# Optimization experiments

Measured on AMD Instinct MI355X. Metric: run time of the kernel, lower is better.

## Reference

```python
import jax, jax.numpy as jnp
import numpy as np

GAMMA = 1.0
INPUT_DIM = 512
NUM_CENTERS = 4096
BATCH = 16384


def setup_inputs() -> dict:
    key = jax.random.key(0)
    kx, kc = jax.random.split(key)
    x = jax.random.normal(kx, (BATCH, INPUT_DIM), dtype=jnp.float32)
    centers = jax.random.normal(kc, (NUM_CENTERS, INPUT_DIM), dtype=jnp.float32)
    return {"x": x, "centers": centers}


def reference(x, centers):
    x_sq = jnp.sum(x * x, axis=-1, keepdims=True)            # [B, 1]
    c_sq = jnp.sum(centers * centers, axis=-1)               # [C]
    cross = jnp.einsum("bd,cd->bc", x, centers)              # [B, C]
    dist_sq = x_sq - 2.0 * cross + c_sq[None, :]
    return jnp.exp(-GAMMA * dist_sq)
```

## Files before the change

### kernel.cpp

```cpp
#include <hip/hip_runtime.h>
#include <stdint.h>

#define M_DIM 16384
#define N_DIM 4096
#define K_DIM 512
#define KB2 1024

#define BM 128
#define BN 256
#define BK 64

typedef __bf16 bf16x8 __attribute__((ext_vector_type(8)));
typedef float f32x16 __attribute__((ext_vector_type(16)));

typedef __attribute__((address_space(3))) uint32_t lds_u32_t;
typedef const __attribute__((address_space(1))) uint32_t glob_u32_t;

__device__ __forceinline__ void gload16(const void* g, void* l) {
    __builtin_amdgcn_global_load_lds((glob_u32_t*)g, (lds_u32_t*)l, 16, 0, 0);
}

__device__ __forceinline__ unsigned pack_bf16(float lo, float hi) {
    return __builtin_amdgcn_perm(__float_as_uint(hi), __float_as_uint(lo), 0x07060302u);
}

__global__ __launch_bounds__(256)
void convert_norm_kernel(const float* __restrict__ src, uint16_t* __restrict__ dst,
                         float* __restrict__ norms, int nrows) {
    const int wave = threadIdx.x >> 6;
    const int lane = threadIdx.x & 63;
    const int row = blockIdx.x * 4 + wave;
    if (row >= nrows) return;
    const float4* p = (const float4*)(src + (size_t)row * K_DIM) + lane * 2;
    float4 a = p[0], b = p[1];
    uint4 u;
    u.x = pack_bf16(a.x, a.y);
    u.y = pack_bf16(a.z, a.w);
    u.z = pack_bf16(b.x, b.y);
    u.w = pack_bf16(b.z, b.w);
    *(uint4*)(dst + (size_t)row * K_DIM + lane * 8) = u;
    float s = a.x*a.x + a.y*a.y + a.z*a.z + a.w*a.w
            + b.x*b.x + b.y*b.y + b.z*b.z + b.w*b.w;
    #pragma unroll
    for (int off = 32; off > 0; off >>= 1) s += __shfl_down(s, off, 64);
    if (lane == 0) norms[row] = s;
}

__global__ __launch_bounds__(256, 2)
void rbf_mfma_kernel(const uint16_t* __restrict__ Abf, const uint16_t* __restrict__ Bbf,
                     const float* __restrict__ xsq, const float* __restrict__ csq,
                     float* __restrict__ out) {
    __shared__ uint16_t As[BM * BK];
    __shared__ uint16_t Bs[BN * BK];

    const int tid  = threadIdx.x;
    const int lane = tid & 63;
    const int wave = tid >> 6;
    const int l31  = lane & 31;
    const int half = lane >> 5;
    const int l7   = lane & 7;

    const int bn = (blockIdx.x & 15) * BN;
    const int bm = (blockIdx.x >> 4) * BM;

    const int wm = (wave >> 1) * 64;
    const int wn = (wave & 1) * 128;

    const int srow   = tid >> 3;
    const int schunk = (tid & 7) ^ (srow & 7);
    const size_t soff = (size_t)srow * KB2 + (size_t)schunk * 16;

    const uint8_t* pA = (const uint8_t*)Abf + (size_t)bm * KB2 + soff;
    const uint8_t* pB = (const uint8_t*)Bbf + (size_t)bn * KB2 + soff;
    uint8_t* AsB = (uint8_t*)As;
    uint8_t* BsB = (uint8_t*)Bs;

    const uint16_t* Arow = As + (wm + l31) * BK;
    const uint16_t* Brow = Bs + (wn + l31) * BK;
    int slot[4];
    #pragma unroll
    for (int ks = 0; ks < 4; ++ks) slot[ks] = (((ks * 2 + half) ^ l7) * 8);

    f32x16 acc[2][4] = {};

    for (int kk = 0; kk < K_DIM / BK; ++kk) {
        #pragma unroll
        for (int t = 0; t < 4; ++t)
            gload16(pA + (size_t)t * 32 * KB2, AsB + t * 4096 + wave * 1024);
        #pragma unroll
        for (int t = 0; t < 8; ++t)
            gload16(pB + (size_t)t * 32 * KB2, BsB + t * 4096 + wave * 1024);
        pA += BK * 2;
        pB += BK * 2;
        __syncthreads();

        #pragma unroll
        for (int ks = 0; ks < 4; ++ks) {
            bf16x8 af[2], bfr[4];
            #pragma unroll
            for (int i = 0; i < 2; ++i)
                af[i] = *(const bf16x8*)(Arow + i * 32 * BK + slot[ks]);
            #pragma unroll
            for (int j = 0; j < 4; ++j)
                bfr[j] = *(const bf16x8*)(Brow + j * 32 * BK + slot[ks]);
            #pragma unroll
            for (int i = 0; i < 2; ++i)
                #pragma unroll
                for (int j = 0; j < 4; ++j)
                    acc[i][j] = __builtin_amdgcn_mfma_f32_32x32x16_bf16(
                        af[i], bfr[j], acc[i][j], 0, 0, 0);
        }
        __syncthreads();
    }

    float cs[4];
    #pragma unroll
    for (int j = 0; j < 4; ++j) cs[j] = csq[bn + wn + 32 * j + l31];

    #pragma unroll
    for (int i = 0; i < 2; ++i) {
        #pragma unroll
        for (int r = 0; r < 16; ++r) {
            const int gm = bm + wm + 32 * i + 4 * half + (r & 3) + 8 * (r >> 2);
            const float xs = xsq[gm];
            float* orow = out + (size_t)gm * N_DIM + bn + wn;
            #pragma unroll
            for (int j = 0; j < 4; ++j) {
                float d = xs - 2.0f * acc[i][j][r] + cs[j];
                orow[32 * j + l31] = __expf(-d);
            }
        }
    }
}

extern "C" void kernel_launch(void* const* d_in, const int* in_sizes, int n_in,
                              void* d_out, int out_size, void* d_ws, size_t ws_size,
                              hipStream_t stream) {
    const float* X = (const float*)d_in[0];
    const float* C = (const float*)d_in[1];
    float* out = (float*)d_out;

    uint16_t* Xbf = (uint16_t*)d_ws;
    uint16_t* Cbf = Xbf + (size_t)M_DIM * K_DIM;
    float* xsq = (float*)(Cbf + (size_t)N_DIM * K_DIM);
    float* csq = xsq + M_DIM;

    convert_norm_kernel<<<M_DIM / 4, 256, 0, stream>>>(X, Xbf, xsq, M_DIM);
    convert_norm_kernel<<<N_DIM / 4, 256, 0, stream>>>(C, Cbf, csq, N_DIM);
    rbf_mfma_kernel<<<(M_DIM / BM) * (N_DIM / BN), 256, 0, stream>>>(Xbf, Cbf, xsq, csq, out);
}
```

Baseline: 343.7 us.

## Switch GEMM operands to FP8 with scaled MFMA and merge conversion kernels

Inputs are converted to FP8 (e4m3) instead of bf16, and the GEMM uses the MI355X scaled f8f6f4 32x32x64 MFMA with unit scales. The K tile grows to 128 with a new rotated LDS swizzle, and the two conversion launches are merged into one. This halves operand bytes and MFMA instruction count, at a large accuracy cost: the cross term x·c is computed from FP8-rounded values and then exponentiated, so errors in dist_sq may exceed tolerance. The kernel is mostly bound by writing the 256MB fp32 output, so GEMM savings matter less.

```diff
diff --git a/kernel.cpp b/kernel.cpp
--- a/kernel.cpp
+++ b/kernel.cpp
@@ -4,13 +4,12 @@
 #define M_DIM 16384
 #define N_DIM 4096
 #define K_DIM 512
-#define KB2 1024
 
 #define BM 128
 #define BN 256
-#define BK 64
+#define BK 128
 
-typedef __bf16 bf16x8 __attribute__((ext_vector_type(8)));
+typedef int v8i __attribute__((ext_vector_type(8)));
 typedef float f32x16 __attribute__((ext_vector_type(16)));
 
 typedef __attribute__((address_space(3))) uint32_t lds_u32_t;
@@ -20,45 +19,48 @@
     __builtin_amdgcn_global_load_lds((glob_u32_t*)g, (lds_u32_t*)l, 16, 0, 0);
 }
 
-__device__ __forceinline__ unsigned pack_bf16(float lo, float hi) {
-    return __builtin_amdgcn_perm(__float_as_uint(hi), __float_as_uint(lo), 0x07060302u);
-}
-
 __global__ __launch_bounds__(256)
-void convert_norm_kernel(const float* __restrict__ src, uint16_t* __restrict__ dst,
-                         float* __restrict__ norms, int nrows) {
+void convert_norm_kernel(const float* __restrict__ X, const float* __restrict__ C,
+                         uint8_t* __restrict__ Xf8, uint8_t* __restrict__ Cf8,
+                         float* __restrict__ xsq, float* __restrict__ csq) {
     const int wave = threadIdx.x >> 6;
     const int lane = threadIdx.x & 63;
     const int row = blockIdx.x * 4 + wave;
-    if (row >= nrows) return;
-    const float4* p = (const float4*)(src + (size_t)row * K_DIM) + lane * 2;
+    const float* src;
+    uint8_t* dst;
+    float* nrm;
+    int r;
+    if (row < M_DIM) { src = X; dst = Xf8; nrm = xsq; r = row; }
+    else             { src = C; dst = Cf8; nrm = csq; r = row - M_DIM; }
+
+    const float4* p = (const float4*)(src + (size_t)r * K_DIM) + lane * 2;
     float4 a = p[0], b = p[1];
-    uint4 u;
-    u.x = pack_bf16(a.x, a.y);
-    u.y = pack_bf16(a.z, a.w);
-    u.z = pack_bf16(b.x, b.y);
-    u.w = pack_bf16(b.z, b.w);
-    *(uint4*)(dst + (size_t)row * K_DIM + lane * 8) = u;
+    uint32_t lo = 0, hi = 0;
+    lo = __builtin_amdgcn_cvt_pk_fp8_f32(a.x, a.y, lo, false);
+    lo = __builtin_amdgcn_cvt_pk_fp8_f32(a.z, a.w, lo, true);
+    hi = __builtin_amdgcn_cvt_pk_fp8_f32(b.x, b.y, hi, false);
+    hi = __builtin_amdgcn_cvt_pk_fp8_f32(b.z, b.w, hi, true);
+    *(uint2*)(dst + (size_t)r * K_DIM + lane * 8) = make_uint2(lo, hi);
+
     float s = a.x*a.x + a.y*a.y + a.z*a.z + a.w*a.w
             + b.x*b.x + b.y*b.y + b.z*b.z + b.w*b.w;
     #pragma unroll
     for (int off = 32; off > 0; off >>= 1) s += __shfl_down(s, off, 64);
-    if (lane == 0) norms[row] = s;
+    if (lane == 0) nrm[r] = s;
 }
 
 __global__ __launch_bounds__(256, 2)
-void rbf_mfma_kernel(const uint16_t* __restrict__ Abf, const uint16_t* __restrict__ Bbf,
+void rbf_mfma_kernel(const uint8_t* __restrict__ A8, const uint8_t* __restrict__ B8,
                      const float* __restrict__ xsq, const float* __restrict__ csq,
                      float* __restrict__ out) {
-    __shared__ uint16_t As[BM * BK];
-    __shared__ uint16_t Bs[BN * BK];
+    __shared__ uint8_t As[BM * BK];
+    __shared__ uint8_t Bs[BN * BK];
 
     const int tid  = threadIdx.x;
     const int lane = tid & 63;
     const int wave = tid >> 6;
-    const int l31  = lane & 31;
-    const int half = lane >> 5;
-    const int l7   = lane & 7;
+    const int h    = lane >> 5;
+    const int r31  = lane & 31;
 
     const int bn = (blockIdx.x & 15) * BN;
     const int bm = (blockIdx.x >> 4) * BM;
@@ -66,68 +68,71 @@
     const int wm = (wave >> 1) * 64;
     const int wn = (wave & 1) * 128;
 
-    const int srow   = tid >> 3;
-    const int schunk = (tid & 7) ^ (srow & 7);
-    const size_t soff = (size_t)srow * KB2 + (size_t)schunk * 16;
-
-    const uint8_t* pA = (const uint8_t*)Abf + (size_t)bm * KB2 + soff;
-    const uint8_t* pB = (const uint8_t*)Bbf + (size_t)bn * KB2 + soff;
-    uint8_t* AsB = (uint8_t*)As;
-    uint8_t* BsB = (uint8_t*)Bs;
-
-    const uint16_t* Arow = As + (wm + l31) * BK;
-    const uint16_t* Brow = Bs + (wn + l31) * BK;
-    int slot[4];
-    #pragma unroll
-    for (int ks = 0; ks < 4; ++ks) slot[ks] = (((ks * 2 + half) ^ l7) * 8);
+    const int sr  = tid >> 3;
+    const int skc = ((tid & 7) - sr) & 7;
+    const uint8_t* pA = A8 + (size_t)(bm + sr) * K_DIM + skc * 16;
+    const uint8_t* pB = B8 + (size_t)(bn + sr) * K_DIM + skc * 16;
+    uint8_t* AsW = As + wave * 1024;
+    uint8_t* BsW = Bs + wave * 1024;
 
     f32x16 acc[2][4] = {};
 
-    for (int kk = 0; kk < K_DIM / BK; ++kk) {
+    for (int k0 = 0; k0 < K_DIM; k0 += BK) {
         #pragma unroll
-        for (int t = 0; t < 4; ++t)
-            gload16(pA + (size_t)t * 32 * KB2, AsB + t * 4096 + wave * 1024);
+        for (int R = 0; R < 4; ++R)
+            gload16(pA + k0 + (size_t)R * 32 * K_DIM, AsW + R * 4096);
         #pragma unroll
-        for (int t = 0; t < 8; ++t)
-            gload16(pB + (size_t)t * 32 * KB2, BsB + t * 4096 + wave * 1024);
-        pA += BK * 2;
-        pB += BK * 2;
+        for (int R = 0; R < 8; ++R)
+            gload16(pB + k0 + (size_t)R * 32 * K_DIM, BsW + R * 4096);
         __syncthreads();
 
         #pragma unroll
-        for (int ks = 0; ks < 4; ++ks) {
-            bf16x8 af[2], bfr[4];
+        for (int ks = 0; ks < 2; ++ks) {
+            v8i av[2], bv[4];
             #pragma unroll
-            for (int i = 0; i < 2; ++i)
-                af[i] = *(const bf16x8*)(Arow + i * 32 * BK + slot[ks]);
+            for (int i = 0; i < 2; ++i) {
+                const int panel = (wm >> 5) + i;
+                uint4 lo = *(const uint4*)(As + (panel * 256 + r31 * 8 + ((ks * 4 + 2 * h + 0 + r31) & 7)) * 16);
+                uint4 hi = *(const uint4*)(As + (panel * 256 + r31 * 8 + ((ks * 4 + 2 * h + 1 + r31) & 7)) * 16);
+                av[i] = (v8i){(int)lo.x, (int)lo.y, (int)lo.z, (int)lo.w,
+                              (int)hi.x, (int)hi.y, (int)hi.z, (int)hi.w};
+            }
             #pragma unroll
-            for (int j = 0; j < 4; ++j)
-                bfr[j] = *(const bf16x8*)(Brow + j * 32 * BK + slot[ks]);
+            for (int j = 0; j < 4; ++j) {
+                const int panel = (wn >> 5) + j;
+                uint4 lo = *(const uint4*)(Bs + (panel * 256 + r31 * 8 + ((ks * 4 + 2 * h + 0 + r31) & 7)) * 16);
+                uint4 hi = *(const uint4*)(Bs + (panel * 256 + r31 * 8 + ((ks * 4 + 2 * h + 1 + r31) & 7)) * 16);
+                bv[j] = (v8i){(int)lo.x, (int)lo.y, (int)lo.z, (int)lo.w,
+                              (int)hi.x, (int)hi.y, (int)hi.z, (int)hi.w};
+            }
             #pragma unroll
             for (int i = 0; i < 2; ++i)
                 #pragma unroll
                 for (int j = 0; j < 4; ++j)
-                    acc[i][j] = __builtin_amdgcn_mfma_f32_32x32x16_bf16(
-                        af[i], bfr[j], acc[i][j], 0, 0, 0);
+                    acc[i][j] = __builtin_amdgcn_mfma_scale_f32_32x32x64_f8f6f4(
+                        av[i], bv[j], acc[i][j],
+                        0 , 0 ,
+                        0, 0x7F7F7F7Fu ,
+                        0, 0x7F7F7F7Fu );
         }
         __syncthreads();
     }
 
     float cs[4];
     #pragma unroll
-    for (int j = 0; j < 4; ++j) cs[j] = csq[bn + wn + 32 * j + l31];
+    for (int j = 0; j < 4; ++j) cs[j] = csq[bn + wn + 32 * j + r31];
 
     #pragma unroll
     for (int i = 0; i < 2; ++i) {
         #pragma unroll
         for (int r = 0; r < 16; ++r) {
-            const int gm = bm + wm + 32 * i + 4 * half + (r & 3) + 8 * (r >> 2);
+            const int gm = bm + wm + 32 * i + 4 * h + (r & 3) + 8 * (r >> 2);
             const float xs = xsq[gm];
             float* orow = out + (size_t)gm * N_DIM + bn + wn;
             #pragma unroll
             for (int j = 0; j < 4; ++j) {
                 float d = xs - 2.0f * acc[i][j][r] + cs[j];
-                orow[32 * j + l31] = __expf(-d);
+                orow[32 * j + r31] = __expf(-d);
             }
         }
     }
@@ -140,12 +145,11 @@
     const float* C = (const float*)d_in[1];
     float* out = (float*)d_out;
 
-    uint16_t* Xbf = (uint16_t*)d_ws;
-    uint16_t* Cbf = Xbf + (size_t)M_DIM * K_DIM;
-    float* xsq = (float*)(Cbf + (size_t)N_DIM * K_DIM);
+    uint8_t* Xf8 = (uint8_t*)d_ws;
+    uint8_t* Cf8 = Xf8 + (size_t)M_DIM * K_DIM;
+    float* xsq = (float*)(Cf8 + (size_t)N_DIM * K_DIM);
     float* csq = xsq + M_DIM;
 
-    convert_norm_kernel<<<M_DIM / 4, 256, 0, stream>>>(X, Xbf, xsq, M_DIM);
-    convert_norm_kernel<<<N_DIM / 4, 256, 0, stream>>>(C, Cbf, csq, N_DIM);
-    rbf_mfma_kernel<<<(M_DIM / BM) * (N_DIM / BN), 256, 0, stream>>>(Xbf, Cbf, xsq, csq, out);
+    convert_norm_kernel<<<(M_DIM + N_DIM) / 4, 256, 0, stream>>>(X, C, Xf8, Cf8, xsq, csq);
+    rbf_mfma_kernel<<<(M_DIM / BM) * (N_DIM / BN), 256, 0, stream>>>(Xf8, Cf8, xsq, csq, out);
 }
```

After: 308.9 us. 1.11x faster.
